# Kernel tuning notes

Hardware: AMD Instinct MI355X
Metric: run time of the kernel (lower is better)

Reference implementation:

```python
import jax, jax.numpy as jnp
import numpy as np

OUT = 4096
IN = 4096
NNZ = 327680
BNNZ = 2048
B = 512

def setup_inputs() -> dict:
    key = jax.random.key(0)
    k1, k2, k3, k4, k5, k6 = jax.random.split(key, 6)
    return {
        "input": jax.random.normal(k1, (B, IN), dtype=jnp.float32),
        "weight_rows": jax.random.randint(k2, (NNZ,), 0, OUT, dtype=jnp.int32),
        "weight_cols": jax.random.randint(k3, (NNZ,), 0, IN, dtype=jnp.int32),
        "weight_values": jax.random.normal(k4, (NNZ,), dtype=jnp.float32),
        "bias_idx": jax.random.randint(k5, (BNNZ,), 0, OUT, dtype=jnp.int32),
        "bias_values": jax.random.normal(k6, (BNNZ,), dtype=jnp.float32),
    }

def reference(input, weight_rows, weight_cols, weight_values, bias_idx, bias_values):
    # COO SpMM: out[b, r] = sum_{k: rows[k]==r} vals[k] * input[b, cols[k]]
    # gather input columns per nnz: [NNZ, B]
    contrib = input[:, weight_cols].T * weight_values[:, None]
    out = jax.ops.segment_sum(contrib, weight_rows, num_segments=OUT)  # [OUT, B]
    out = out.T  # [B, OUT]
    # sparse bias -> dense (duplicate indices summed, matching coalesce())
    bias = jnp.zeros((OUT,), dtype=bias_values.dtype).at[bias_idx].add(bias_values)
    return out + bias[None, :]
```

## Files before the change

kernel.cpp:

```cpp
#include <hip/hip_runtime.h>

#define OUT_DIM 4096
#define IN_DIM 4096
#define NNZ 327680
#define BNNZ 2048
#define BATCH 512
#define NCHK 64
#define CNNZ (NNZ / NCHK)
#define SMAX 160
#define RT 16
#define TT 512

typedef int   i2 __attribute__((ext_vector_type(2)));
typedef float f4 __attribute__((ext_vector_type(4)));

__device__ __forceinline__ unsigned short f2bf(float f) {
    unsigned int x = __float_as_uint(f);
    x += 0x7fffu + ((x >> 16) & 1u);
    return (unsigned short)(x >> 16);
}

union PrepSMem {
    struct { float tile[4][32][33]; } a;
    struct { int h[OUT_DIM]; int s[1024]; int2 sl[CNNZ]; } b;
};

__global__ __launch_bounds__(1024)
void prep_k(const float* __restrict__ in, unsigned short* __restrict__ inputT,
            const int* __restrict__ rows, const int* __restrict__ cols,
            const float* __restrict__ vals,
            int* __restrict__ lrp, int2* __restrict__ slots) {
    __shared__ PrepSMem u;
    const int bid = blockIdx.x, t = threadIdx.x;
    if (bid >= NCHK) {
        const int g = t >> 8, tx = t & 31, ty = (t >> 5) & 7;
        const int job = (bid - NCHK) * 4 + g;
        const int bx = (job & 127) << 5;
        const int by = (job >> 7) << 5;
        for (int i = ty; i < 32; i += 8)
            u.a.tile[g][i][tx] = in[(size_t)(by + i) * IN_DIM + bx + tx];
        __syncthreads();
        for (int i = ty; i < 32; i += 8)
            inputT[(size_t)(bx + i) * BATCH + by + tx] = f2bf(u.a.tile[g][tx][i]);
    } else {
        const int c = bid;
        const int base = c * CNNZ;
#pragma unroll
        for (int i = 0; i < 4; ++i) u.b.h[i * 1024 + t] = 0;
        __syncthreads();
#pragma unroll
        for (int i = 0; i < CNNZ / 1024; ++i)
            atomicAdd(&u.b.h[rows[base + i * 1024 + t]], 1);
        __syncthreads();
        const int c0 = u.b.h[4 * t], c1 = u.b.h[4 * t + 1];
        const int c2 = u.b.h[4 * t + 2], c3 = u.b.h[4 * t + 3];
        const int sum = c0 + c1 + c2 + c3;
        u.b.s[t] = sum;
        __syncthreads();
        for (int d = 1; d < 1024; d <<= 1) {
            const int v = (t >= d) ? u.b.s[t - d] : 0;
            __syncthreads();
            u.b.s[t] += v;
            __syncthreads();
        }
        const int e0 = u.b.s[t] - sum, e1 = e0 + c0, e2 = e1 + c1, e3 = e2 + c2;
        u.b.h[4 * t] = e0; u.b.h[4 * t + 1] = e1;
        u.b.h[4 * t + 2] = e2; u.b.h[4 * t + 3] = e3;
        int* lc = lrp + (size_t)c * 4097;
        lc[4 * t] = e0; lc[4 * t + 1] = e1; lc[4 * t + 2] = e2; lc[4 * t + 3] = e3;
        if (t == 1023) lc[4096] = CNNZ;
        __syncthreads();
#pragma unroll
        for (int i = 0; i < CNNZ / 1024; ++i) {
            const int k = base + i * 1024 + t;
            const int r = rows[k];
            const int p = atomicAdd(&u.b.h[r], 1);
            u.b.sl[p] = make_int2(cols[k] * (BATCH * 2),
                                  __float_as_int(vals[k]));
        }
        __syncthreads();
#pragma unroll
        for (int i = 0; i < CNNZ / 1024; ++i)
            slots[base + i * 1024 + t] = u.b.sl[i * 1024 + t];
    }
}

__global__ __launch_bounds__(1024, 4)
void spmm_k(const unsigned short* __restrict__ inputT, const int* __restrict__ lrp,
            const int2* __restrict__ slots, const int* __restrict__ b_idx,
            const float* __restrict__ b_vals, float* __restrict__ out) {
    const int w = threadIdx.x >> 6;
    const int lane = threadIdx.x & 63;
    const int r0 = blockIdx.x * RT;
    const int r = r0 + w;

    __shared__ int2  s_slot[RT][SMAX];
    __shared__ float tile[RT][BATCH];
    __shared__ float bias_l[RT];

    if (threadIdx.x < RT) bias_l[threadIdx.x] = 0.f;
    __syncthreads();

    const int* lc = lrp + (size_t)lane * 4097;
    const int beg = lc[r];
    const int cnt = lc[r + 1] - beg;
    int x = cnt;
#pragma unroll
    for (int d = 1; d < 64; d <<= 1) {
        const int y = __shfl_up(x, d, 64);
        if (lane >= d) x += y;
    }
    const int excl = x - cnt;
    int total = __shfl(x, 63, 64);
    total = min(total, SMAX);
    for (int j = 0; j < cnt; ++j) {
        const int p = excl + j;
        if (p < SMAX) {
            i2 sv = __builtin_nontemporal_load(
                reinterpret_cast<const i2*>(&slots[lane * CNNZ + beg + j]));
            s_slot[w][p] = make_int2(sv.x, sv.y);
        }
    }

#pragma unroll
    for (int i = 0; i < 2; ++i) {
        const int ii = threadIdx.x * 2 + i;
        const int d = b_idx[ii] - r0;
        if ((unsigned)d < RT) atomicAdd(&bias_l[d], b_vals[ii]);
    }

    const char* base = (const char*)inputT + lane * 16;
    float a0 = 0.f, a1 = 0.f, a2 = 0.f, a3 = 0.f;
    float a4 = 0.f, a5 = 0.f, a6 = 0.f, a7 = 0.f;
#pragma unroll 4
    for (int j = 0; j < total; ++j) {
        const int2 sv = s_slot[w][j];
        const uint4 q = *reinterpret_cast<const uint4*>(base + sv.x);
        const float v = __int_as_float(sv.y);
        a0 = fmaf(v, __uint_as_float(q.x << 16), a0);
        a1 = fmaf(v, __uint_as_float(q.x & 0xffff0000u), a1);
        a2 = fmaf(v, __uint_as_float(q.y << 16), a2);
        a3 = fmaf(v, __uint_as_float(q.y & 0xffff0000u), a3);
        a4 = fmaf(v, __uint_as_float(q.z << 16), a4);
        a5 = fmaf(v, __uint_as_float(q.z & 0xffff0000u), a5);
        a6 = fmaf(v, __uint_as_float(q.w << 16), a6);
        a7 = fmaf(v, __uint_as_float(q.w & 0xffff0000u), a7);
    }
    float4* tp = reinterpret_cast<float4*>(&tile[w][lane * 8]);
    tp[0] = make_float4(a0, a1, a2, a3);
    tp[1] = make_float4(a4, a5, a6, a7);
    __syncthreads();

    const int rq = (threadIdx.x & 3) * 4;
    const float4 bv = make_float4(bias_l[rq + 0], bias_l[rq + 1],
                                  bias_l[rq + 2], bias_l[rq + 3]);
#pragma unroll
    for (int k2 = 0; k2 < 2; ++k2) {
        const int b = (threadIdx.x >> 2) + k2 * 256;
        f4 o = {tile[rq + 0][b] + bv.x, tile[rq + 1][b] + bv.y,
                tile[rq + 2][b] + bv.z, tile[rq + 3][b] + bv.w};
        __builtin_nontemporal_store(o, reinterpret_cast<f4*>(
            &out[(size_t)b * OUT_DIM + r0 + rq]));
    }
}

extern "C" void kernel_launch(void* const* d_in, const int* in_sizes, int n_in,
                              void* d_out, int out_size, void* d_ws, size_t ws_size,
                              hipStream_t stream) {
    const float* input   = (const float*)d_in[0];
    const int*   w_rows  = (const int*)d_in[1];
    const int*   w_cols  = (const int*)d_in[2];
    const float* w_vals  = (const float*)d_in[3];
    const int*   b_idx   = (const int*)d_in[4];
    const float* b_vals  = (const float*)d_in[5];
    float* out = (float*)d_out;

    char* ws = (char*)d_ws;
    const size_t MB = (size_t)1024 * 1024;
    unsigned short* inputT = (unsigned short*)ws;
    int*   lrp   = (int*)(ws + 4 * MB);
    int2*  slots = (int2*)(ws + 6 * MB);

    prep_k<<<NCHK + TT, 1024, 0, stream>>>(input, inputT, w_rows, w_cols, w_vals,
                                           lrp, slots);

    spmm_k<<<OUT_DIM / RT, 1024, 0, stream>>>(inputT, lrp, slots, b_idx, b_vals,
                                              out);
}
```

Before: 37.68 us.

## Split each row across two waves and use wave-shuffle scan in prep

```diff
diff --git a/kernel.cpp b/kernel.cpp
--- a/kernel.cpp
+++ b/kernel.cpp
@@ -8,7 +8,7 @@
 #define NCHK 64
 #define CNNZ (NNZ / NCHK)
 #define SMAX 160
-#define RT 16
+#define RT 8
 #define TT 512
 
 typedef int   i2 __attribute__((ext_vector_type(2)));
@@ -22,7 +22,7 @@
 
 union PrepSMem {
     struct { float tile[4][32][33]; } a;
-    struct { int h[OUT_DIM]; int s[1024]; int2 sl[CNNZ]; } b;
+    struct { int h[OUT_DIM]; int ws[16]; int2 sl[CNNZ]; } b;
 };
 
 __global__ __launch_bounds__(1024)
@@ -45,6 +45,7 @@
     } else {
         const int c = bid;
         const int base = c * CNNZ;
+        const int lane = t & 63, wv = t >> 6;
 #pragma unroll
         for (int i = 0; i < 4; ++i) u.b.h[i * 1024 + t] = 0;
         __syncthreads();
@@ -55,15 +56,27 @@
         const int c0 = u.b.h[4 * t], c1 = u.b.h[4 * t + 1];
         const int c2 = u.b.h[4 * t + 2], c3 = u.b.h[4 * t + 3];
         const int sum = c0 + c1 + c2 + c3;
-        u.b.s[t] = sum;
-        __syncthreads();
-        for (int d = 1; d < 1024; d <<= 1) {
-            const int v = (t >= d) ? u.b.s[t - d] : 0;
-            __syncthreads();
-            u.b.s[t] += v;
-            __syncthreads();
-        }
-        const int e0 = u.b.s[t] - sum, e1 = e0 + c0, e2 = e1 + c1, e3 = e2 + c2;
+        int x = sum;
+#pragma unroll
+        for (int d = 1; d < 64; d <<= 1) {
+            const int y = __shfl_up(x, d, 64);
+            if (lane >= d) x += y;
+        }
+        if (lane == 63) u.b.ws[wv] = x;
+        __syncthreads();
+        if (t < 16) {
+            const int v = u.b.ws[t];
+            int xx = v;
+#pragma unroll
+            for (int d = 1; d < 16; d <<= 1) {
+                const int y = __shfl_up(xx, d, 64);
+                if (t >= d) xx += y;
+            }
+            u.b.ws[t] = xx - v;
+        }
+        __syncthreads();
+        const int e0 = u.b.ws[wv] + (x - sum);
+        const int e1 = e0 + c0, e2 = e1 + c1, e3 = e2 + c2;
         u.b.h[4 * t] = e0; u.b.h[4 * t + 1] = e1;
         u.b.h[4 * t + 2] = e2; u.b.h[4 * t + 3] = e3;
         int* lc = lrp + (size_t)c * 4097;
@@ -85,14 +98,16 @@
     }
 }
 
-__global__ __launch_bounds__(1024, 4)
+__global__ __launch_bounds__(1024, 8)
 void spmm_k(const unsigned short* __restrict__ inputT, const int* __restrict__ lrp,
             const int2* __restrict__ slots, const int* __restrict__ b_idx,
             const float* __restrict__ b_vals, float* __restrict__ out) {
     const int w = threadIdx.x >> 6;
+    const int h = w & 1;
+    const int w2 = w >> 1;
     const int lane = threadIdx.x & 63;
     const int r0 = blockIdx.x * RT;
-    const int r = r0 + w;
+    const int r = r0 + w2;
 
     __shared__ int2  s_slot[RT][SMAX];
     __shared__ float tile[RT][BATCH];
@@ -113,12 +128,15 @@
     const int excl = x - cnt;
     int total = __shfl(x, 63, 64);
     total = min(total, SMAX);
+    const int halfc = total >> 1;
+    const int jbeg = h ? halfc : 0;
+    const int jend = h ? total : halfc;
     for (int j = 0; j < cnt; ++j) {
         const int p = excl + j;
-        if (p < SMAX) {
+        if (p >= jbeg && p < jend) {
             i2 sv = __builtin_nontemporal_load(
                 reinterpret_cast<const i2*>(&slots[lane * CNNZ + beg + j]));
-            s_slot[w][p] = make_int2(sv.x, sv.y);
+            s_slot[w2][p] = make_int2(sv.x, sv.y);
         }
     }
 
@@ -133,8 +151,8 @@
     float a0 = 0.f, a1 = 0.f, a2 = 0.f, a3 = 0.f;
     float a4 = 0.f, a5 = 0.f, a6 = 0.f, a7 = 0.f;
 #pragma unroll 4
-    for (int j = 0; j < total; ++j) {
-        const int2 sv = s_slot[w][j];
+    for (int j = jbeg; j < jend; ++j) {
+        const int2 sv = s_slot[w2][j];
         const uint4 q = *reinterpret_cast<const uint4*>(base + sv.x);
         const float v = __int_as_float(sv.y);
         a0 = fmaf(v, __uint_as_float(q.x << 16), a0);
@@ -146,22 +164,25 @@
         a6 = fmaf(v, __uint_as_float(q.w << 16), a6);
         a7 = fmaf(v, __uint_as_float(q.w & 0xffff0000u), a7);
     }
-    float4* tp = reinterpret_cast<float4*>(&tile[w][lane * 8]);
-    tp[0] = make_float4(a0, a1, a2, a3);
-    tp[1] = make_float4(a4, a5, a6, a7);
+    float* tp = &tile[w2][lane * 8];
+    if (h == 0) {
+        tp[0] = a0; tp[1] = a1; tp[2] = a2; tp[3] = a3;
+        tp[4] = a4; tp[5] = a5; tp[6] = a6; tp[7] = a7;
+    }
     __syncthreads();
-
-    const int rq = (threadIdx.x & 3) * 4;
+    if (h == 1) {
+        tp[0] += a0; tp[1] += a1; tp[2] += a2; tp[3] += a3;
+        tp[4] += a4; tp[5] += a5; tp[6] += a6; tp[7] += a7;
+    }
+    __syncthreads();
+
+    const int rq = (threadIdx.x & 1) * 4;
+    const int bl = threadIdx.x >> 1;
     const float4 bv = make_float4(bias_l[rq + 0], bias_l[rq + 1],
                                   bias_l[rq + 2], bias_l[rq + 3]);
-#pragma unroll
-    for (int k2 = 0; k2 < 2; ++k2) {
-        const int b = (threadIdx.x >> 2) + k2 * 256;
-        f4 o = {tile[rq + 0][b] + bv.x, tile[rq + 1][b] + bv.y,
-                tile[rq + 2][b] + bv.z, tile[rq + 3][b] + bv.w};
-        __builtin_nontemporal_store(o, reinterpret_cast<f4*>(
-            &out[(size_t)b * OUT_DIM + r0 + rq]));
-    }
+    float4 o = make_float4(tile[rq + 0][bl] + bv.x, tile[rq + 1][bl] + bv.y,
+                           tile[rq + 2][bl] + bv.z, tile[rq + 3][bl] + bv.w);
+    *reinterpret_cast<float4*>(&out[(size_t)bl * OUT_DIM + r0 + rq]) = o;
 }
 
 extern "C" void kernel_launch(void* const* d_in, const int* in_sizes, int n_in,
```

Result: slower. 39.17 us (+3.9%).
